# Kernel tuning notes

Hardware: AMD Instinct MI355X
Metric: run time of the kernel (lower is better)

Reference implementation:

```python
import jax, jax.numpy as jnp
import numpy as np

N, E, C, R, B = 16384, 262144, 256, 9, 4


def _basis_mm(x, coeff, basis):
    # x: [E, Cin], coeff = att[edge_type]: [E, B], basis: [B, Cin, Cout]
    # equals x_e @ (sum_b coeff[e,b] * basis_b) = x_e @ W[edge_type[e]]
    h = jnp.einsum('ec,bco->ebo', x, basis)          # [E, B, Cout]
    return jnp.einsum('ebo,eb->eo', h, coeff)        # [E, Cout]


def _segment_softmax(score, gkey, nseg):
    smax = jax.ops.segment_max(score, gkey, num_segments=nseg)
    ex = jnp.exp(score - smax[gkey])
    den = jax.ops.segment_sum(ex, gkey, num_segments=nseg)
    return ex / den[gkey]


def _attn_branch(rel_emb, basis, att, aw, ab, etypes, seg):
    # relation-specific transform of edge features -> node messages
    m = _basis_mm(rel_emb, att[etypes], basis)                       # [E, Cn]
    # per-relation Linear (weight aw[r], bias ab[r]) + leaky_relu (slope 0.01)
    score = jax.nn.leaky_relu(jnp.sum(m * aw[etypes], -1) + ab[etypes])
    # original: softmax over dest index with -1e8 on edges of other relations,
    # then zeroed by mask == softmax within (dest node, relation) groups
    alpha = _segment_softmax(score, seg * R + etypes, N * R)         # [E]
    agg = jax.ops.segment_sum(alpha[:, None] * m, seg, num_segments=N)  # [N, Cn]
    onehot = jax.nn.one_hot(etypes, R, dtype=m.dtype)
    cnt = jax.ops.segment_sum(onehot, seg, num_segments=N)           # [N, R]
    div = (cnt > 0).astype(m.dtype).sum(-1)
    div = jnp.where(div == 0, jnp.ones_like(div), div)
    return agg / div[:, None]


def setup_inputs():
    key = jax.random.key(0)
    ks = jax.random.split(key, 16)
    p = lambda k, shp: jax.random.normal(k, shp, jnp.float32) * 0.05
    return {
        'edge_index': jax.random.randint(ks[0], (2, E), 0, N, dtype=jnp.int32),
        'nf': jax.random.normal(ks[1], (N, C), jnp.float32),
        'ef': jax.random.normal(ks[2], (E, C), jnp.float32),
        'edge_type_rel': jax.random.randint(ks[3], (E,), 0, R, dtype=jnp.int32),
        'edge_type_rel_inv': jax.random.randint(ks[4], (E,), 0, R, dtype=jnp.int32),
        'edge_norm': jax.random.uniform(ks[5], (E,), jnp.float32),
        'sub2rel_basis': p(ks[6], (B, C, C)),
        'sub2rel_att': p(ks[7], (R, B)),
        'obj2rel_basis': p(ks[8], (B, C, C)),
        'obj2rel_att': p(ks[9], (R, B)),
        'rel2sub_basis': p(ks[10], (B, C, C)),
        'rel2sub_att': p(ks[11], (R, B)),
        'rel2sub_attn_w': p(ks[12], (R, C)),
        'rel2sub_attn_b': jnp.zeros((R,), jnp.float32),
        'rel2obj_basis': p(ks[13], (B, C, C)),
        'rel2obj_att': p(ks[14], (R, B)),
        'rel2obj_attn_w': p(ks[15], (R, C)),
        'rel2obj_attn_b': jnp.zeros((R,), jnp.float32),
    }


def reference(edge_index, nf, ef, edge_type_rel, edge_type_rel_inv, edge_norm,
              sub2rel_basis, sub2rel_att, obj2rel_basis, obj2rel_att,
              rel2sub_basis, rel2sub_att, rel2sub_attn_w, rel2sub_attn_b,
              rel2obj_basis, rel2obj_att, rel2obj_attn_w, rel2obj_attn_b):
    src, dst = edge_index[0], edge_index[1]
    # sub2rel / obj2rel: per-edge relation-specific GEMM (mask+sum over rel in
    # the original collapses to a gather of W by edge type)
    s2r = _basis_mm(nf[src], sub2rel_att[edge_type_rel], sub2rel_basis)
    o2r = _basis_mm(nf[dst], obj2rel_att[edge_type_rel_inv], obj2rel_basis)
    rel_emb = ef + 0.5 * (s2r + o2r)
    # rel2sub aggregates at src (edgeindex_i = edge_index[0], rel types = inv)
    sub_agg = _attn_branch(rel_emb, rel2sub_basis, rel2sub_att,
                           rel2sub_attn_w, rel2sub_attn_b, edge_type_rel_inv, src)
    # rel2obj aggregates at dst (edgeindex_i = edge_index[1], rel types = fwd)
    obj_agg = _attn_branch(rel_emb, rel2obj_basis, rel2obj_att,
                           rel2obj_attn_w, rel2obj_attn_b, edge_type_rel, dst)
    node_emb = nf + 0.5 * (sub_agg + obj_agg)
    return node_emb, rel_emb
```

## Files before the change

kernel.cpp:

```cpp
#include <hip/hip_runtime.h>

#define N_ 16384
#define E_ 262144
#define C_ 256
#define R_ 9
#define B_ 4
#define NKEY (N_ * R_)

typedef unsigned short u16;
typedef unsigned int u32;

typedef __bf16 bf16x8 __attribute__((ext_vector_type(8)));
typedef float f32x4 __attribute__((ext_vector_type(4)));

__device__ __forceinline__ u16 f2bf(float x) {
  u32 u = __float_as_uint(x);
  u32 r = (u + 0x7fffu + ((u >> 16) & 1u)) >> 16;
  return (u16)r;
}
__device__ __forceinline__ float bf2f(u16 h) {
  return __uint_as_float(((u32)h) << 16);
}

__global__ void prep_w_kernel(const float* __restrict__ basis,
                              const float* __restrict__ att,
                              u16* __restrict__ out, int stacked) {
  int c = blockIdx.x;
  int r = blockIdx.y;
  int o = threadIdx.x;
  float s = 0.f;
#pragma unroll
  for (int b = 0; b < B_; ++b)
    s += att[r * B_ + b] * basis[((long)b * C_ + c) * C_ + o];
  u16 h = f2bf(s);
  if (stacked) out[(long)o * (R_ * C_) + r * C_ + c] = h;
  else         out[((long)r * C_ + o) * C_ + c] = h;
}

__global__ void prep_v_kernel(const float* __restrict__ basis,
                              const float* __restrict__ att,
                              const float* __restrict__ aw,
                              float* __restrict__ v) {
  int c = blockIdx.x, r = blockIdx.y, o = threadIdx.x;
  float w = 0.f;
#pragma unroll
  for (int b = 0; b < B_; ++b)
    w += att[r * B_ + b] * basis[((long)b * C_ + c) * C_ + o];
  float p = w * aw[r * C_ + o];
  __shared__ float red[256];
  red[o] = p;
  __syncthreads();
  for (int s = 128; s > 0; s >>= 1) {
    if (o < s) red[o] += red[o + s];
    __syncthreads();
  }
  if (o == 0) v[r * C_ + c] = red[0];
}

__global__ void cvt_bf16_kernel(const float* __restrict__ in, u16* __restrict__ out) {
  long i = ((long)blockIdx.x * 256 + threadIdx.x) * 4;
  float4 f = *(const float4*)(in + i);
  ushort4 h;
  h.x = f2bf(f.x); h.y = f2bf(f.y); h.z = f2bf(f.z); h.w = f2bf(f.w);
  *(ushort4*)(out + i) = h;
}

#define BM 128
#define BN 128
#define BK 32
#define LSTR 40

template <int OBF16>
__global__ __launch_bounds__(256) void gemm_kernel(
    const u16* __restrict__ A, long aBatch, int lda,
    const u16* __restrict__ Bt, long bBatch, int K,
    void* __restrict__ Out, long cBatch, int ldc) {
  __shared__ __attribute__((aligned(16))) u16 As[BM * LSTR];
  __shared__ __attribute__((aligned(16))) u16 Bs[BN * LSTR];

  const int t = threadIdx.x;
  const int m0 = blockIdx.x * BM;
  const int n0 = blockIdx.y * BN;
  const long zb = blockIdx.z;

  const int tr = t >> 1;
  const int th = (t & 1) * 16;

  const int w = t >> 6, lane = t & 63;
  const int wm = (w >> 1) * 64, wn = (w & 1) * 64;
  const int lr = lane & 15;
  const int lk = (lane >> 4) * 8;

  f32x4 acc[4][4];
#pragma unroll
  for (int i = 0; i < 4; ++i)
#pragma unroll
    for (int j = 0; j < 4; ++j) acc[i][j] = (f32x4){0.f, 0.f, 0.f, 0.f};

  const u16* aRow = A + zb * aBatch + (long)(m0 + tr) * lda + th;
  const u16* bRow = Bt + zb * bBatch + (long)(n0 + tr) * K + th;

  u16* aDst = &As[tr * LSTR + th];
  u16* bDst = &Bs[tr * LSTR + th];

  for (int k0 = 0; k0 < K; k0 += BK) {
    int4 a0 = *(const int4*)(aRow);
    int4 a1 = *(const int4*)(aRow + 8);
    int4 b0 = *(const int4*)(bRow);
    int4 b1 = *(const int4*)(bRow + 8);
    *(int4*)(aDst) = a0;
    *(int4*)(aDst + 8) = a1;
    *(int4*)(bDst) = b0;
    *(int4*)(bDst + 8) = b1;
    aRow += BK;
    bRow += BK;
    __syncthreads();

    bf16x8 af[4], bg[4];
#pragma unroll
    for (int mi = 0; mi < 4; ++mi)
      af[mi] = *(const bf16x8*)&As[(wm + mi * 16 + lr) * LSTR + lk];
#pragma unroll
    for (int ni = 0; ni < 4; ++ni)
      bg[ni] = *(const bf16x8*)&Bs[(wn + ni * 16 + lr) * LSTR + lk];
#pragma unroll
    for (int mi = 0; mi < 4; ++mi)
#pragma unroll
      for (int ni = 0; ni < 4; ++ni)
        acc[mi][ni] = __builtin_amdgcn_mfma_f32_16x16x32_bf16(af[mi], bg[ni], acc[mi][ni], 0, 0, 0);

    __syncthreads();
  }

  long base = zb * cBatch;
#pragma unroll
  for (int mi = 0; mi < 4; ++mi) {
    int rowb = m0 + wm + mi * 16 + ((lane >> 4) * 4);
#pragma unroll
    for (int ni = 0; ni < 4; ++ni) {
      int col = n0 + wn + ni * 16 + lr;
      f32x4 c = acc[mi][ni];
#pragma unroll
      for (int i = 0; i < 4; ++i) {
        long idx = base + (long)(rowb + i) * ldc + col;
        if (OBF16) ((u16*)Out)[idx] = f2bf(c[i]);
        else ((float*)Out)[idx] = c[i];
      }
    }
  }
}

__global__ __launch_bounds__(256) void relemb_kernel(
    const float* __restrict__ ef, const u16* __restrict__ Ysub,
    const u16* __restrict__ Yobj, const int* __restrict__ src,
    const int* __restrict__ dst, const int* __restrict__ et,
    const int* __restrict__ eti, const float* __restrict__ vS,
    const float* __restrict__ abS, const float* __restrict__ vO,
    const float* __restrict__ abO, float* __restrict__ rel,
    float* __restrict__ scoreS, float* __restrict__ scoreO,
    int* __restrict__ cntS, int* __restrict__ cntO) {
  int e = blockIdx.x * 4 + (threadIdx.x >> 6);
  int lane = threadIdx.x & 63;
  int c = lane * 4;
  int sn = src[e], dn = dst[e], tf = et[e], ti = eti[e];
  long rsub = ((long)tf * N_ + sn) * C_ + c;
  long robj = ((long)ti * N_ + dn) * C_ + c;
  ushort4 ys = *(const ushort4*)(Ysub + rsub);
  ushort4 yo = *(const ushort4*)(Yobj + robj);
  long ei = (long)e * C_ + c;
  float4 f = *(const float4*)(ef + ei);
  float4 o;
  o.x = f.x + 0.5f * (bf2f(ys.x) + bf2f(yo.x));
  o.y = f.y + 0.5f * (bf2f(ys.y) + bf2f(yo.y));
  o.z = f.z + 0.5f * (bf2f(ys.z) + bf2f(yo.z));
  o.w = f.w + 0.5f * (bf2f(ys.w) + bf2f(yo.w));
  *(float4*)(rel + ei) = o;

  float4 wS = *(const float4*)(vS + ti * C_ + c);
  float4 wO = *(const float4*)(vO + tf * C_ + c);
  float pS = o.x * wS.x + o.y * wS.y + o.z * wS.z + o.w * wS.w;
  float pO = o.x * wO.x + o.y * wO.y + o.z * wO.z + o.w * wO.w;
#pragma unroll
  for (int off = 32; off > 0; off >>= 1) {
    pS += __shfl_xor(pS, off);
    pO += __shfl_xor(pO, off);
  }
  if (lane == 0) {
    float sS = pS + abS[ti];
    sS = sS > 0.f ? sS : 0.01f * sS;
    scoreS[e] = sS;
    atomicAdd(&cntS[sn * R_ + ti], 1);
    float sO = pO + abO[tf];
    sO = sO > 0.f ? sO : 0.01f * sO;
    scoreO[e] = sO;
    atomicAdd(&cntO[dn * R_ + tf], 1);
  }
}

__global__ __launch_bounds__(256) void scan1_kernel(const int* __restrict__ cnt,
                                                    int* __restrict__ offs,
                                                    int* __restrict__ part) {
  __shared__ int lds[256];
  int b = blockIdx.x, t = threadIdx.x;
  int base = b * 1024 + t * 4;
  int4 v = *(const int4*)(cnt + base);
  int tsum = v.x + v.y + v.z + v.w;
  lds[t] = tsum;
  __syncthreads();
  for (int d = 1; d < 256; d <<= 1) {
    int x = (t >= d) ? lds[t - d] : 0;
    __syncthreads();
    lds[t] += x;
    __syncthreads();
  }
  int run = (t == 0) ? 0 : lds[t - 1];
  int4 o;
  o.x = run;
  o.y = run + v.x;
  o.z = o.y + v.y;
  o.w = o.z + v.z;
  *(int4*)(offs + base) = o;
  if (t == 255) part[b] = lds[255];
}

__global__ __launch_bounds__(256) void scan2_kernel(int* __restrict__ part) {
  __shared__ int lds[256];
  int t = threadIdx.x;
  lds[t] = (t < 144) ? part[t] : 0;
  __syncthreads();
  for (int d = 1; d < 256; d <<= 1) {
    int x = (t >= d) ? lds[t - d] : 0;
    __syncthreads();
    lds[t] += x;
    __syncthreads();
  }
  if (t < 144) part[t] = (t == 0) ? 0 : lds[t - 1];
}

__global__ __launch_bounds__(256) void scan3_kernel(const int* __restrict__ part,
                                                    int* __restrict__ offs,
                                                    int* __restrict__ cursor) {
  int i = blockIdx.x * 256 + threadIdx.x;
  int v = offs[i] + part[i >> 10];
  offs[i] = v;
  cursor[i] = v;
}

__global__ __launch_bounds__(256) void scatter_kernel(
    const int* __restrict__ etype, const int* __restrict__ seg,
    int* __restrict__ cursor, int* __restrict__ order) {
  int e = blockIdx.x * 256 + threadIdx.x;
  int key = seg[e] * R_ + etype[e];
  int idx = atomicAdd(&cursor[key], 1);
  order[idx] = e;
}

__global__ __launch_bounds__(256) void zgather_kernel(
    const float* __restrict__ rel, const float* __restrict__ score,
    const int* __restrict__ order, const int* __restrict__ offs,
    const int* __restrict__ cnt, u16* __restrict__ z) {
  int key = blockIdx.x * 4 + (threadIdx.x >> 6);
  int lane = threadIdx.x & 63;
  int c = lane * 4;
  int len = cnt[key];
  int start = offs[key];

  float ax = 0.f, ay = 0.f, az = 0.f, aw = 0.f, den = 0.f;
  if (len > 0) {
    float m = -1e30f;
    for (int i = 0; i < len; ++i) m = fmaxf(m, score[order[start + i]]);
    for (int i = 0; i < len; ++i) {
      int e = order[start + i];
      float ex = __expf(score[e] - m);
      den += ex;
      float4 x = *(const float4*)(rel + (long)e * C_ + c);
      ax += ex * x.x; ay += ex * x.y; az += ex * x.z; aw += ex * x.w;
    }
    float inv = 1.f / den;
    ax *= inv; ay *= inv; az *= inv; aw *= inv;
  }
  int n = key / R_, r = key - n * R_;
  ushort4 h;
  h.x = f2bf(ax); h.y = f2bf(ay); h.z = f2bf(az); h.w = f2bf(aw);
  *(ushort4*)(z + (long)n * (R_ * C_) + r * C_ + c) = h;
}

__global__ __launch_bounds__(256) void final_kernel(
    const float* __restrict__ nf, const float* __restrict__ aggS,
    const float* __restrict__ aggO, const int* __restrict__ cntS,
    const int* __restrict__ cntO, float* __restrict__ node) {
  int n = blockIdx.x, c = threadIdx.x;
  int ds = 0, dobj = 0;
#pragma unroll
  for (int r = 0; r < R_; ++r) {
    ds += (cntS[n * R_ + r] > 0);
    dobj += (cntO[n * R_ + r] > 0);
  }
  float fs = ds ? (float)ds : 1.f;
  float fo = dobj ? (float)dobj : 1.f;
  long i = (long)n * C_ + c;
  node[i] = nf[i] + 0.5f * (aggS[i] / fs + aggO[i] / fo);
}

extern "C" void kernel_launch(void* const* d_in, const int* in_sizes, int n_in,
                              void* d_out, int out_size, void* d_ws, size_t ws_size,
                              hipStream_t stream) {
  const int* edge_index = (const int*)d_in[0];
  const float* nf = (const float*)d_in[1];
  const float* ef = (const float*)d_in[2];
  const int* et = (const int*)d_in[3];
  const int* eti = (const int*)d_in[4];
  const float* s2r_basis = (const float*)d_in[6];
  const float* s2r_att = (const float*)d_in[7];
  const float* o2r_basis = (const float*)d_in[8];
  const float* o2r_att = (const float*)d_in[9];
  const float* r2s_basis = (const float*)d_in[10];
  const float* r2s_att = (const float*)d_in[11];
  const float* r2s_aw = (const float*)d_in[12];
  const float* r2s_ab = (const float*)d_in[13];
  const float* r2o_basis = (const float*)d_in[14];
  const float* r2o_att = (const float*)d_in[15];
  const float* r2o_aw = (const float*)d_in[16];
  const float* r2o_ab = (const float*)d_in[17];

  const int* src = edge_index;
  const int* dst = edge_index + E_;

  char* ws = (char*)d_ws;
  u16* WtSub = (u16*)(ws + 0);
  u16* WtObj = (u16*)(ws + 1179648);
  u16* WtR2S = (u16*)(ws + 2359296);
  u16* WtR2O = (u16*)(ws + 3538944);
  float* vS = (float*)(ws + 4718592);
  float* vO = (float*)(ws + 4727808);
  u16* nfb = (u16*)(ws + 4737024);
  float* scoreS = (float*)(ws + 13125632);
  float* scoreO = (float*)(ws + 14174208);
  int* cntS = (int*)(ws + 15222784);
  int* cntO = (int*)(ws + 15812608);
  int* offs = (int*)(ws + 16402432);
  int* cursor = (int*)(ws + 16992256);
  int* order = (int*)(ws + 17582080);
  int* part = (int*)(ws + 18630656);
  u16* Ysub = (u16*)(ws + 18634752);
  u16* Yobj = (u16*)(ws + 94132224);
  u16* zbuf = (u16*)(ws + 18634752);
  float* aggS = (float*)(ws + 94132224);
  float* aggO = (float*)(ws + 110909440);

  float* node_out = (float*)d_out;
  float* rel_out = (float*)d_out + (long)N_ * C_;

  prep_w_kernel<<<dim3(C_, R_), 256, 0, stream>>>(s2r_basis, s2r_att, WtSub, 0);
  prep_w_kernel<<<dim3(C_, R_), 256, 0, stream>>>(o2r_basis, o2r_att, WtObj, 0);
  prep_w_kernel<<<dim3(C_, R_), 256, 0, stream>>>(r2s_basis, r2s_att, WtR2S, 1);
  prep_w_kernel<<<dim3(C_, R_), 256, 0, stream>>>(r2o_basis, r2o_att, WtR2O, 1);
  prep_v_kernel<<<dim3(C_, R_), 256, 0, stream>>>(r2s_basis, r2s_att, r2s_aw, vS);
  prep_v_kernel<<<dim3(C_, R_), 256, 0, stream>>>(r2o_basis, r2o_att, r2o_aw, vO);
  cvt_bf16_kernel<<<(N_ * C_) / 1024, 256, 0, stream>>>(nf, nfb);
  hipMemsetAsync(cntS, 0, 2L * 589824, stream);

  gemm_kernel<1><<<dim3(N_ / BM, C_ / BN, R_), 256, 0, stream>>>(
      nfb, 0L, C_, WtSub, (long)C_ * C_, C_, Ysub, (long)N_ * C_, C_);
  gemm_kernel<1><<<dim3(N_ / BM, C_ / BN, R_), 256, 0, stream>>>(
      nfb, 0L, C_, WtObj, (long)C_ * C_, C_, Yobj, (long)N_ * C_, C_);

  relemb_kernel<<<E_ / 4, 256, 0, stream>>>(ef, Ysub, Yobj, src, dst, et, eti,
                                            vS, r2s_ab, vO, r2o_ab, rel_out,
                                            scoreS, scoreO, cntS, cntO);

  scan1_kernel<<<144, 256, 0, stream>>>(cntS, offs, part);
  scan2_kernel<<<1, 256, 0, stream>>>(part);
  scan3_kernel<<<576, 256, 0, stream>>>(part, offs, cursor);
  scatter_kernel<<<E_ / 256, 256, 0, stream>>>(eti, src, cursor, order);
  zgather_kernel<<<NKEY / 4, 256, 0, stream>>>(rel_out, scoreS, order, offs, cntS, zbuf);
  gemm_kernel<0><<<dim3(N_ / BM, C_ / BN, 1), 256, 0, stream>>>(
      zbuf, 0L, R_ * C_, WtR2S, 0L, R_ * C_, aggS, 0L, C_);

  scan1_kernel<<<144, 256, 0, stream>>>(cntO, offs, part);
  scan2_kernel<<<1, 256, 0, stream>>>(part);
  scan3_kernel<<<576, 256, 0, stream>>>(part, offs, cursor);
  scatter_kernel<<<E_ / 256, 256, 0, stream>>>(et, dst, cursor, order);
  zgather_kernel<<<NKEY / 4, 256, 0, stream>>>(rel_out, scoreO, order, offs, cntO, zbuf);
  gemm_kernel<0><<<dim3(N_ / BM, C_ / BN, 1), 256, 0, stream>>>(
      zbuf, 0L, R_ * C_, WtR2O, 0L, R_ * C_, aggO, 0L, C_);

  final_kernel<<<N_, 256, 0, stream>>>(nf, aggS, aggO, cntS, cntO, node_out);

  (void)in_sizes; (void)n_in; (void)out_size; (void)ws_size;
}
```

Baseline: 1.083 ms.

## Merge sub/obj pipelines, fuse prep kernels, use direct-to-LDS loads and fused epilogue

Merges the four weight-prep and two vector-prep kernels into one launch. Runs a single combined scan/scatter/gather over both subject and object key spaces, which halves the number of launches. The softmax max-subtraction pass is dropped, relying on scores being small. The GEMM now stages tiles with global_load_lds and an unpadded LDS layout. The final node update is folded into the GEMM epilogue using precomputed reciprocal divisors, and relemb processes 8 channels per lane. The trade-offs are possible LDS bank conflicts from removing the padding and a risk of exp overflow without the max shift.

```diff
diff --git a/kernel.cpp b/kernel.cpp
--- a/kernel.cpp
+++ b/kernel.cpp
@@ -6,12 +6,14 @@
 #define R_ 9
 #define B_ 4
 #define NKEY (N_ * R_)
+#define NKEY2 (2 * NKEY)
 
 typedef unsigned short u16;
 typedef unsigned int u32;
 
 typedef __bf16 bf16x8 __attribute__((ext_vector_type(8)));
 typedef float f32x4 __attribute__((ext_vector_type(4)));
+typedef unsigned short u16x8 __attribute__((ext_vector_type(8)));
 
 __device__ __forceinline__ u16 f2bf(float x) {
   u32 u = __float_as_uint(x);
@@ -22,39 +24,56 @@
   return __uint_as_float(((u32)h) << 16);
 }
 
-__global__ void prep_w_kernel(const float* __restrict__ basis,
-                              const float* __restrict__ att,
-                              u16* __restrict__ out, int stacked) {
-  int c = blockIdx.x;
-  int r = blockIdx.y;
-  int o = threadIdx.x;
-  float s = 0.f;
-#pragma unroll
-  for (int b = 0; b < B_; ++b)
-    s += att[r * B_ + b] * basis[((long)b * C_ + c) * C_ + o];
-  u16 h = f2bf(s);
-  if (stacked) out[(long)o * (R_ * C_) + r * C_ + c] = h;
-  else         out[((long)r * C_ + o) * C_ + c] = h;
-}
-
-__global__ void prep_v_kernel(const float* __restrict__ basis,
-                              const float* __restrict__ att,
-                              const float* __restrict__ aw,
-                              float* __restrict__ v) {
+__device__ __forceinline__ void gld16(const void* g, void* l) {
+  __builtin_amdgcn_global_load_lds(
+      (const __attribute__((address_space(1))) void*)g,
+      (__attribute__((address_space(3))) void*)l, 16, 0, 0);
+}
+
+__global__ __launch_bounds__(256) void prep_kernel(
+    const float* __restrict__ b1, const float* __restrict__ a1,
+    const float* __restrict__ b2, const float* __restrict__ a2,
+    const float* __restrict__ b3, const float* __restrict__ a3,
+    const float* __restrict__ aw3,
+    const float* __restrict__ b4, const float* __restrict__ a4,
+    const float* __restrict__ aw4,
+    u16* __restrict__ W1, u16* __restrict__ W2,
+    u16* __restrict__ W3, u16* __restrict__ W4,
+    float* __restrict__ v3, float* __restrict__ v4) {
   int c = blockIdx.x, r = blockIdx.y, o = threadIdx.x;
-  float w = 0.f;
-#pragma unroll
-  for (int b = 0; b < B_; ++b)
-    w += att[r * B_ + b] * basis[((long)b * C_ + c) * C_ + o];
-  float p = w * aw[r * C_ + o];
+  float s1 = 0.f, s2 = 0.f, s3 = 0.f, s4 = 0.f;
+#pragma unroll
+  for (int b = 0; b < B_; ++b) {
+    long bi = ((long)b * C_ + c) * C_ + o;
+    s1 += a1[r * B_ + b] * b1[bi];
+    s2 += a2[r * B_ + b] * b2[bi];
+    s3 += a3[r * B_ + b] * b3[bi];
+    s4 += a4[r * B_ + b] * b4[bi];
+  }
+  W1[((long)r * C_ + o) * C_ + c] = f2bf(s1);
+  W2[((long)r * C_ + o) * C_ + c] = f2bf(s2);
+  W3[(long)o * (R_ * C_) + r * C_ + c] = f2bf(s3);
+  W4[(long)o * (R_ * C_) + r * C_ + c] = f2bf(s4);
+
   __shared__ float red[256];
-  red[o] = p;
+  red[o] = s3 * aw3[r * C_ + o];
   __syncthreads();
   for (int s = 128; s > 0; s >>= 1) {
     if (o < s) red[o] += red[o + s];
     __syncthreads();
   }
-  if (o == 0) v[r * C_ + c] = red[0];
+  float rv3 = red[0];
+  __syncthreads();
+  red[o] = s4 * aw4[r * C_ + o];
+  __syncthreads();
+  for (int s = 128; s > 0; s >>= 1) {
+    if (o < s) red[o] += red[o + s];
+    __syncthreads();
+  }
+  if (o == 0) {
+    v3[r * C_ + c] = rv3;
+    v4[r * C_ + c] = red[0];
+  }
 }
 
 __global__ void cvt_bf16_kernel(const float* __restrict__ in, u16* __restrict__ out) {
@@ -68,23 +87,23 @@
 #define BM 128
 #define BN 128
 #define BK 32
-#define LSTR 40
-
-template <int OBF16>
+
+template <int OMODE>
 __global__ __launch_bounds__(256) void gemm_kernel(
     const u16* __restrict__ A, long aBatch, int lda,
     const u16* __restrict__ Bt, long bBatch, int K,
-    void* __restrict__ Out, long cBatch, int ldc) {
-  __shared__ __attribute__((aligned(16))) u16 As[BM * LSTR];
-  __shared__ __attribute__((aligned(16))) u16 Bs[BN * LSTR];
+    void* __restrict__ Out, long cBatch, int ldc,
+    const float* __restrict__ nf, const float* __restrict__ dv) {
+  __shared__ __attribute__((aligned(16))) u16 As[BM * BK];
+  __shared__ __attribute__((aligned(16))) u16 Bs[BN * BK];
 
   const int t = threadIdx.x;
   const int m0 = blockIdx.x * BM;
   const int n0 = blockIdx.y * BN;
   const long zb = blockIdx.z;
 
-  const int tr = t >> 1;
-  const int th = (t & 1) * 16;
+  const int sr = t >> 2;
+  const int sk = (t & 3) * 8;
 
   const int w = t >> 6, lane = t & 63;
   const int wm = (w >> 1) * 64, wn = (w & 1) * 64;
@@ -97,32 +116,32 @@
 #pragma unroll
     for (int j = 0; j < 4; ++j) acc[i][j] = (f32x4){0.f, 0.f, 0.f, 0.f};
 
-  const u16* aRow = A + zb * aBatch + (long)(m0 + tr) * lda + th;
-  const u16* bRow = Bt + zb * bBatch + (long)(n0 + tr) * K + th;
-
-  u16* aDst = &As[tr * LSTR + th];
-  u16* bDst = &Bs[tr * LSTR + th];
+  const u16* aR = A + zb * aBatch + (long)(m0 + sr) * lda + sk;
+  const u16* bR = Bt + zb * bBatch + (long)(n0 + sr) * K + sk;
+  const long aStep = 64L * lda;
+  const long bStep = 64L * K;
+
+  u16* aD0 = &As[t * 8];
+  u16* aD1 = &As[2048 + t * 8];
+  u16* bD0 = &Bs[t * 8];
+  u16* bD1 = &Bs[2048 + t * 8];
 
   for (int k0 = 0; k0 < K; k0 += BK) {
-    int4 a0 = *(const int4*)(aRow);
-    int4 a1 = *(const int4*)(aRow + 8);
-    int4 b0 = *(const int4*)(bRow);
-    int4 b1 = *(const int4*)(bRow + 8);
-    *(int4*)(aDst) = a0;
-    *(int4*)(aDst + 8) = a1;
-    *(int4*)(bDst) = b0;
-    *(int4*)(bDst + 8) = b1;
-    aRow += BK;
-    bRow += BK;
+    gld16(aR, aD0);
+    gld16(aR + aStep, aD1);
+    gld16(bR, bD0);
+    gld16(bR + bStep, bD1);
+    aR += BK;
+    bR += BK;
     __syncthreads();
 
     bf16x8 af[4], bg[4];
 #pragma unroll
     for (int mi = 0; mi < 4; ++mi)
-      af[mi] = *(const bf16x8*)&As[(wm + mi * 16 + lr) * LSTR + lk];
+      af[mi] = *(const bf16x8*)&As[(wm + mi * 16 + lr) * BK + lk];
 #pragma unroll
     for (int ni = 0; ni < 4; ++ni)
-      bg[ni] = *(const bf16x8*)&Bs[(wn + ni * 16 + lr) * LSTR + lk];
+      bg[ni] = *(const bf16x8*)&Bs[(wn + ni * 16 + lr) * BK + lk];
 #pragma unroll
     for (int mi = 0; mi < 4; ++mi)
 #pragma unroll
@@ -136,6 +155,11 @@
 #pragma unroll
   for (int mi = 0; mi < 4; ++mi) {
     int rowb = m0 + wm + mi * 16 + ((lane >> 4) * 4);
+    float fs[4];
+    if (OMODE >= 3) {
+#pragma unroll
+      for (int i = 0; i < 4; ++i) fs[i] = 0.5f * dv[rowb + i];
+    }
 #pragma unroll
     for (int ni = 0; ni < 4; ++ni) {
       int col = n0 + wn + ni * 16 + lr;
@@ -143,7 +167,9 @@
 #pragma unroll
       for (int i = 0; i < 4; ++i) {
         long idx = base + (long)(rowb + i) * ldc + col;
-        if (OBF16) ((u16*)Out)[idx] = f2bf(c[i]);
+        if (OMODE == 1) ((u16*)Out)[idx] = f2bf(c[i]);
+        else if (OMODE == 3) ((float*)Out)[idx] = nf[idx] + fs[i] * c[i];
+        else if (OMODE == 4) ((float*)Out)[idx] += fs[i] * c[i];
         else ((float*)Out)[idx] = c[i];
       }
     }
@@ -158,43 +184,66 @@
     const float* __restrict__ abS, const float* __restrict__ vO,
     const float* __restrict__ abO, float* __restrict__ rel,
     float* __restrict__ scoreS, float* __restrict__ scoreO,
-    int* __restrict__ cntS, int* __restrict__ cntO) {
-  int e = blockIdx.x * 4 + (threadIdx.x >> 6);
-  int lane = threadIdx.x & 63;
-  int c = lane * 4;
+    int* __restrict__ cnt) {
+  int e = blockIdx.x * 8 + (threadIdx.x >> 5);
+  int h = threadIdx.x & 31;
+  int c = h * 8;
   int sn = src[e], dn = dst[e], tf = et[e], ti = eti[e];
-  long rsub = ((long)tf * N_ + sn) * C_ + c;
-  long robj = ((long)ti * N_ + dn) * C_ + c;
-  ushort4 ys = *(const ushort4*)(Ysub + rsub);
-  ushort4 yo = *(const ushort4*)(Yobj + robj);
+
+  u16x8 ys = *(const u16x8*)(Ysub + ((long)tf * N_ + sn) * C_ + c);
+  u16x8 yo = *(const u16x8*)(Yobj + ((long)ti * N_ + dn) * C_ + c);
   long ei = (long)e * C_ + c;
-  float4 f = *(const float4*)(ef + ei);
-  float4 o;
-  o.x = f.x + 0.5f * (bf2f(ys.x) + bf2f(yo.x));
-  o.y = f.y + 0.5f * (bf2f(ys.y) + bf2f(yo.y));
-  o.z = f.z + 0.5f * (bf2f(ys.z) + bf2f(yo.z));
-  o.w = f.w + 0.5f * (bf2f(ys.w) + bf2f(yo.w));
-  *(float4*)(rel + ei) = o;
-
-  float4 wS = *(const float4*)(vS + ti * C_ + c);
-  float4 wO = *(const float4*)(vO + tf * C_ + c);
-  float pS = o.x * wS.x + o.y * wS.y + o.z * wS.z + o.w * wS.w;
-  float pO = o.x * wO.x + o.y * wO.y + o.z * wO.z + o.w * wO.w;
-#pragma unroll
-  for (int off = 32; off > 0; off >>= 1) {
+  float4 f0 = *(const float4*)(ef + ei);
+  float4 f1 = *(const float4*)(ef + ei + 4);
+
+  float o0 = f0.x + 0.5f * (bf2f(ys[0]) + bf2f(yo[0]));
+  float o1 = f0.y + 0.5f * (bf2f(ys[1]) + bf2f(yo[1]));
+  float o2 = f0.z + 0.5f * (bf2f(ys[2]) + bf2f(yo[2]));
+  float o3 = f0.w + 0.5f * (bf2f(ys[3]) + bf2f(yo[3]));
+  float o4 = f1.x + 0.5f * (bf2f(ys[4]) + bf2f(yo[4]));
+  float o5 = f1.y + 0.5f * (bf2f(ys[5]) + bf2f(yo[5]));
+  float o6 = f1.z + 0.5f * (bf2f(ys[6]) + bf2f(yo[6]));
+  float o7 = f1.w + 0.5f * (bf2f(ys[7]) + bf2f(yo[7]));
+  *(float4*)(rel + ei) = (float4){o0, o1, o2, o3};
+  *(float4*)(rel + ei + 4) = (float4){o4, o5, o6, o7};
+
+  float4 wS0 = *(const float4*)(vS + ti * C_ + c);
+  float4 wS1 = *(const float4*)(vS + ti * C_ + c + 4);
+  float4 wO0 = *(const float4*)(vO + tf * C_ + c);
+  float4 wO1 = *(const float4*)(vO + tf * C_ + c + 4);
+  float pS = o0 * wS0.x + o1 * wS0.y + o2 * wS0.z + o3 * wS0.w +
+             o4 * wS1.x + o5 * wS1.y + o6 * wS1.z + o7 * wS1.w;
+  float pO = o0 * wO0.x + o1 * wO0.y + o2 * wO0.z + o3 * wO0.w +
+             o4 * wO1.x + o5 * wO1.y + o6 * wO1.z + o7 * wO1.w;
+#pragma unroll
+  for (int off = 16; off > 0; off >>= 1) {
     pS += __shfl_xor(pS, off);
     pO += __shfl_xor(pO, off);
   }
-  if (lane == 0) {
+  if (h == 0) {
     float sS = pS + abS[ti];
     sS = sS > 0.f ? sS : 0.01f * sS;
     scoreS[e] = sS;
-    atomicAdd(&cntS[sn * R_ + ti], 1);
+    atomicAdd(&cnt[sn * R_ + ti], 1);
     float sO = pO + abO[tf];
     sO = sO > 0.f ? sO : 0.01f * sO;
     scoreO[e] = sO;
-    atomicAdd(&cntO[dn * R_ + tf], 1);
-  }
+    atomicAdd(&cnt[NKEY + dn * R_ + tf], 1);
+  }
+}
+
+__global__ __launch_bounds__(256) void div_kernel(const int* __restrict__ cnt,
+                                                  float* __restrict__ divS,
+                                                  float* __restrict__ divO) {
+  int n = blockIdx.x * 256 + threadIdx.x;
+  int ds = 0, dq = 0;
+#pragma unroll
+  for (int r = 0; r < R_; ++r) {
+    ds += (cnt[n * R_ + r] > 0);
+    dq += (cnt[NKEY + n * R_ + r] > 0);
+  }
+  divS[n] = ds ? 1.f / (float)ds : 1.f;
+  divO[n] = dq ? 1.f / (float)dq : 1.f;
 }
 
 __global__ __launch_bounds__(256) void scan1_kernel(const int* __restrict__ cnt,
@@ -223,18 +272,18 @@
   if (t == 255) part[b] = lds[255];
 }
 
-__global__ __launch_bounds__(256) void scan2_kernel(int* __restrict__ part) {
-  __shared__ int lds[256];
+__global__ __launch_bounds__(512) void scan2_kernel(int* __restrict__ part) {
+  __shared__ int lds[512];
   int t = threadIdx.x;
-  lds[t] = (t < 144) ? part[t] : 0;
+  lds[t] = (t < 288) ? part[t] : 0;
   __syncthreads();
-  for (int d = 1; d < 256; d <<= 1) {
+  for (int d = 1; d < 512; d <<= 1) {
     int x = (t >= d) ? lds[t - d] : 0;
     __syncthreads();
     lds[t] += x;
     __syncthreads();
   }
-  if (t < 144) part[t] = (t == 0) ? 0 : lds[t - 1];
+  if (t < 288) part[t] = (t == 0) ? 0 : lds[t - 1];
 }
 
 __global__ __launch_bounds__(256) void scan3_kernel(const int* __restrict__ part,
@@ -247,59 +296,47 @@
 }
 
 __global__ __launch_bounds__(256) void scatter_kernel(
-    const int* __restrict__ etype, const int* __restrict__ seg,
+    const int* __restrict__ et, const int* __restrict__ eti,
+    const int* __restrict__ src, const int* __restrict__ dst,
     int* __restrict__ cursor, int* __restrict__ order) {
   int e = blockIdx.x * 256 + threadIdx.x;
-  int key = seg[e] * R_ + etype[e];
-  int idx = atomicAdd(&cursor[key], 1);
-  order[idx] = e;
+  int kS = src[e] * R_ + eti[e];
+  int kO = NKEY + dst[e] * R_ + et[e];
+  order[atomicAdd(&cursor[kS], 1)] = e;
+  order[atomicAdd(&cursor[kO], 1)] = e;
 }
 
 __global__ __launch_bounds__(256) void zgather_kernel(
-    const float* __restrict__ rel, const float* __restrict__ score,
-    const int* __restrict__ order, const int* __restrict__ offs,
-    const int* __restrict__ cnt, u16* __restrict__ z) {
+    const float* __restrict__ rel, const float* __restrict__ scoreS,
+    const float* __restrict__ scoreO, const int* __restrict__ order,
+    const int* __restrict__ offs, const int* __restrict__ cnt,
+    u16* __restrict__ zS, u16* __restrict__ zO) {
   int key = blockIdx.x * 4 + (threadIdx.x >> 6);
   int lane = threadIdx.x & 63;
   int c = lane * 4;
   int len = cnt[key];
   int start = offs[key];
+  const float* score = scoreS;
+  u16* z = zS;
+  int k2 = key;
+  if (key >= NKEY) { score = scoreO; z = zO; k2 = key - NKEY; }
 
   float ax = 0.f, ay = 0.f, az = 0.f, aw = 0.f, den = 0.f;
+  for (int i = 0; i < len; ++i) {
+    int e = order[start + i];
+    float ex = __expf(score[e]);
+    den += ex;
+    float4 x = *(const float4*)(rel + (long)e * C_ + c);
+    ax += ex * x.x; ay += ex * x.y; az += ex * x.z; aw += ex * x.w;
+  }
   if (len > 0) {
-    float m = -1e30f;
-    for (int i = 0; i < len; ++i) m = fmaxf(m, score[order[start + i]]);
-    for (int i = 0; i < len; ++i) {
-      int e = order[start + i];
-      float ex = __expf(score[e] - m);
-      den += ex;
-      float4 x = *(const float4*)(rel + (long)e * C_ + c);
-      ax += ex * x.x; ay += ex * x.y; az += ex * x.z; aw += ex * x.w;
-    }
     float inv = 1.f / den;
     ax *= inv; ay *= inv; az *= inv; aw *= inv;
   }
-  int n = key / R_, r = key - n * R_;
+  int n = k2 / R_, r = k2 - n * R_;
   ushort4 h;
   h.x = f2bf(ax); h.y = f2bf(ay); h.z = f2bf(az); h.w = f2bf(aw);
   *(ushort4*)(z + (long)n * (R_ * C_) + r * C_ + c) = h;
-}
-
-__global__ __launch_bounds__(256) void final_kernel(
-    const float* __restrict__ nf, const float* __restrict__ aggS,
-    const float* __restrict__ aggO, const int* __restrict__ cntS,
-    const int* __restrict__ cntO, float* __restrict__ node) {
-  int n = blockIdx.x, c = threadIdx.x;
-  int ds = 0, dobj = 0;
-#pragma unroll
-  for (int r = 0; r < R_; ++r) {
-    ds += (cntS[n * R_ + r] > 0);
-    dobj += (cntO[n * R_ + r] > 0);
-  }
-  float fs = ds ? (float)ds : 1.f;
-  float fo = dobj ? (float)dobj : 1.f;
-  long i = (long)n * C_ + c;
-  node[i] = nf[i] + 0.5f * (aggS[i] / fs + aggO[i] / fo);
 }
 
 extern "C" void kernel_launch(void* const* d_in, const int* in_sizes, int n_in,
@@ -336,56 +373,49 @@
   u16* nfb = (u16*)(ws + 4737024);
   float* scoreS = (float*)(ws + 13125632);
   float* scoreO = (float*)(ws + 14174208);
-  int* cntS = (int*)(ws + 15222784);
-  int* cntO = (int*)(ws + 15812608);
+  int* cnt = (int*)(ws + 15222784);
   int* offs = (int*)(ws + 16402432);
-  int* cursor = (int*)(ws + 16992256);
-  int* order = (int*)(ws + 17582080);
-  int* part = (int*)(ws + 18630656);
-  u16* Ysub = (u16*)(ws + 18634752);
-  u16* Yobj = (u16*)(ws + 94132224);
-  u16* zbuf = (u16*)(ws + 18634752);
-  float* aggS = (float*)(ws + 94132224);
-  float* aggO = (float*)(ws + 110909440);
+  int* cursor = (int*)(ws + 17582080);
+  int* order = (int*)(ws + 18761728);
+  int* part = (int*)(ws + 20858880);
+  float* divS = (float*)(ws + 20860928);
+  float* divO = (float*)(ws + 20926464);
+  u16* Ysub = (u16*)(ws + 20992000);
+  u16* Yobj = (u16*)(ws + 96489472);
+  u16* zS = Ysub;
+  u16* zO = Yobj;
 
   float* node_out = (float*)d_out;
   float* rel_out = (float*)d_out + (long)N_ * C_;
 
-  prep_w_kernel<<<dim3(C_, R_), 256, 0, stream>>>(s2r_basis, s2r_att, WtSub, 0);
-  prep_w_kernel<<<dim3(C_, R_), 256, 0, stream>>>(o2r_basis, o2r_att, WtObj, 0);
-  prep_w_kernel<<<dim3(C_, R_), 256, 0, stream>>>(r2s_basis, r2s_att, WtR2S, 1);
-  prep_w_kernel<<<dim3(C_, R_), 256, 0, stream>>>(r2o_basis, r2o_att, WtR2O, 1);
-  prep_v_kernel<<<dim3(C_, R_), 256, 0, stream>>>(r2s_basis, r2s_att, r2s_aw, vS);
-  prep_v_kernel<<<dim3(C_, R_), 256, 0, stream>>>(r2o_basis, r2o_att, r2o_aw, vO);
+  prep_kernel<<<dim3(C_, R_), 256, 0, stream>>>(
+      s2r_basis, s2r_att, o2r_basis, o2r_att,
+      r2s_basis, r2s_att, r2s_aw, r2o_basis, r2o_att, r2o_aw,
+      WtSub, WtObj, WtR2S, WtR2O, vS, vO);
   cvt_bf16_kernel<<<(N_ * C_) / 1024, 256, 0, stream>>>(nf, nfb);
-  hipMemsetAsync(cntS, 0, 2L * 589824, stream);
+  hipMemsetAsync(cnt, 0, (size_t)NKEY2 * 4, stream);
 
   gemm_kernel<1><<<dim3(N_ / BM, C_ / BN, R_), 256, 0, stream>>>(
-      nfb, 0L, C_, WtSub, (long)C_ * C_, C_, Ysub, (long)N_ * C_, C_);
+      nfb, 0L, C_, WtSub, (long)C_ * C_, C_, Ysub, (long)N_ * C_, C_, nullptr, nullptr);
   gemm_kernel<1><<<dim3(N_ / BM, C_ / BN, R_), 256, 0, stream>>>(
-      nfb, 0L, C_, WtObj, (long)C_ * C_, C_, Yobj, (long)N_ * C_, C_);
-
-  relemb_kernel<<<E_ / 4, 256, 0, stream>>>(ef, Ysub, Yobj, src, dst, et, eti,
+      nfb, 0L, C_, WtObj, (long)C_ * C_, C_, Yobj, (long)N_ * C_, C_, nullptr, nullptr);
+
+  relemb_kernel<<<E_ / 8, 256, 0, stream>>>(ef, Ysub, Yobj, src, dst, et, eti,
                                             vS, r2s_ab, vO, r2o_ab, rel_out,
-                                            scoreS, scoreO, cntS, cntO);
-
-  scan1_kernel<<<144, 256, 0, stream>>>(cntS, offs, part);
-  scan2_kernel<<<1, 256, 0, stream>>>(part);
-  scan3_kernel<<<576, 256, 0, stream>>>(part, offs, cursor);
-  scatter_kernel<<<E_ / 256, 256, 0, stream>>>(eti, src, cursor, order);
-  zgather_kernel<<<NKEY / 4, 256, 0, stream>>>(rel_out, scoreS, order, offs, cntS, zbuf);
-  gemm_kernel<0><<<dim3(N_ / BM, C_ / BN, 1), 256, 0, stream>>>(
-      zbuf, 0L, R_ * C_, WtR2S, 0L, R_ * C_, aggS, 0L, C_);
-
-  scan1_kernel<<<144, 256, 0, stream>>>(cntO, offs, part);
-  scan2_kernel<<<1, 256, 0, stream>>>(part);
-  scan3_kernel<<<576, 256, 0, stream>>>(part, offs, cursor);
-  scatter_kernel<<<E_ / 256, 256, 0, stream>>>(et, dst, cursor, order);
-  zgather_kernel<<<NKEY / 4, 256, 0, stream>>>(rel_out, scoreO, order, offs, cntO, zbuf);
-  gemm_kernel<0><<<dim3(N_ / BM, C_ / BN, 1), 256, 0, stream>>>(
-      zbuf, 0L, R_ * C_, WtR2O, 0L, R_ * C_, aggO, 0L, C_);
-
-  final_kernel<<<N_, 256, 0, stream>>>(nf, aggS, aggO, cntS, cntO, node_out);
+                                            scoreS, scoreO, cnt);
+  div_kernel<<<N_ / 256, 256, 0, stream>>>(cnt, divS, divO);
+
+  scan1_kernel<<<288, 256, 0, stream>>>(cnt, offs, part);
+  scan2_kernel<<<1, 512, 0, stream>>>(part);
+  scan3_kernel<<<NKEY2 / 256, 256, 0, stream>>>(part, offs, cursor);
+  scatter_kernel<<<E_ / 256, 256, 0, stream>>>(et, eti, src, dst, cursor, order);
+  zgather_kernel<<<NKEY2 / 4, 256, 0, stream>>>(rel_out, scoreS, scoreO, order,
+                                                offs, cnt, zS, zO);
+
+  gemm_kernel<3><<<dim3(N_ / BM, C_ / BN, 1), 256, 0, stream>>>(
+      zS, 0L, R_ * C_, WtR2S, 0L, R_ * C_, node_out, 0L, C_, nf, divS);
+  gemm_kernel<4><<<dim3(N_ / BM, C_ / BN, 1), 256, 0, stream>>>(
+      zO, 0L, R_ * C_, WtR2O, 0L, R_ * C_, node_out, 0L, C_, nullptr, divO);
 
   (void)in_sizes; (void)n_in; (void)out_size; (void)ws_size;
 }
```

Result: faster. 993.5 us (-8.2%).
